# Performance work log

Hardware: AMD Instinct MI355X
Metric: run time of the kernel (lower is better)

## Reference

```python
import jax, jax.numpy as jnp
import numpy as np

B, S, DIM, H, HD = 2, 2048, 512, 8, 64
VD = DIM // H  # 64
QK = H * HD


def setup_inputs() -> dict:
    key = jax.random.key(0)
    k1, k2, k3, k4, k5 = jax.random.split(key, 5)
    x = jax.random.normal(k1, (B, S, DIM), dtype=jnp.float32)
    mask = jax.random.bernoulli(k2, 0.5, (B, S))
    # per-position rotation matrices, scaled to keep activations O(1)
    rotator = jax.random.normal(k3, (B, S, HD, HD), dtype=jnp.float32) / np.sqrt(HD)
    # torch Linear weights: [out_features, in_features], no bias
    W_trans = jax.random.normal(k4, (2 * QK + DIM, DIM), dtype=jnp.float32) / np.sqrt(DIM)
    W_o = jax.random.normal(k5, (DIM, DIM), dtype=jnp.float32) / np.sqrt(DIM)
    return {"x": x, "mask": mask, "rotator": rotator, "W_trans": W_trans, "W_o": W_o}


def _taylor_attention(qs, ks, vs, mask):
    # 2nd-order Taylor approximation of exp for softmax weights
    # qs/ks: [B,S,H,HD], vs: [B,S,H,VD], mask: [B,S] key mask
    scores = jnp.einsum('bqhd,bkhd->bhqk', qs, ks) / np.sqrt(HD)
    w = 1.0 + scores + 0.5 * scores * scores
    w = jnp.where(mask[:, None, None, :], w, 0.0)
    w = w / jnp.sum(w, axis=-1, keepdims=True)
    out = jnp.einsum('bhqk,bkhd->bqhd', w, vs)
    return out.reshape(out.shape[0], out.shape[1], -1)  # [B,S,DIM]


def reference(x, mask, rotator, W_trans, W_o):
    t = x @ W_trans.T  # [B,S,2*QK+DIM]
    qs = t[..., :QK].reshape(B, S, H, HD)
    ks = t[..., QK:2 * QK].reshape(B, S, H, HD)
    vs = t[..., 2 * QK:].reshape(B, S, H, VD)
    sel = mask[..., None, None]
    qs = jnp.where(sel, jnp.einsum('bsij,bshj->bshi', rotator, qs), qs)
    ks = jnp.where(sel, jnp.einsum('bsij,bshj->bshi', rotator, ks), ks)
    out = _taylor_attention(qs, ks, vs, mask)
    return out @ W_o.T
```

## Files before the change

kernel.cpp:

```cpp
#include <hip/hip_runtime.h>
#include <hip/hip_bf16.h>

#define B_    2
#define S_    2048
#define DIM_  512
#define H_    8
#define HD_   64
#define TOUT_ 1536
#define ROWS_ (B_ * S_)

typedef unsigned short ushort_t;
typedef __attribute__((ext_vector_type(8))) __bf16 bf16x8;
typedef __attribute__((ext_vector_type(4))) float floatx4;

#define AS_GLB __attribute__((address_space(1)))
#define AS_LDS __attribute__((address_space(3)))

__device__ __forceinline__ unsigned short f2bfu(float f) {
    unsigned u = __float_as_uint(f);
    unsigned r = (u + 0x7fffu + ((u >> 16) & 1u)) >> 16;
    return (unsigned short)r;
}
__device__ __forceinline__ bf16x8 cvt8(const float* p) {
    float4 a = *reinterpret_cast<const float4*>(p);
    float4 b = *reinterpret_cast<const float4*>(p + 4);
    ushort_t o[8] = {f2bfu(a.x), f2bfu(a.y), f2bfu(a.z), f2bfu(a.w),
                     f2bfu(b.x), f2bfu(b.y), f2bfu(b.z), f2bfu(b.w)};
    return *reinterpret_cast<bf16x8*>(o);
}

#define XN4_  (ROWS_ * DIM_ / 4)
#define WTN4_ (TOUT_ * DIM_ / 4)
#define WON4_ (DIM_ * DIM_ / 4)
#define CASTBLKS_ ((XN4_ + WTN4_ + WON4_) / 256)
__global__ __launch_bounds__(256) void prep_inputs(const float* __restrict__ x,
                                                   const float* __restrict__ wt,
                                                   const float* __restrict__ wo,
                                                   const unsigned char* __restrict__ mb,
                                                   ushort_t* __restrict__ xb,
                                                   ushort_t* __restrict__ wtb,
                                                   ushort_t* __restrict__ wob,
                                                   int* __restrict__ wm) {
    if (blockIdx.x >= CASTBLKS_) {
        __shared__ int s_bf, s_f, s_u8;
        int tid = threadIdx.x;
        if (tid == 0) { s_bf = 0; s_f = 0; s_u8 = 0; }
        __syncthreads();
        int cbf = 0, cf = 0, cu8 = 0;
        for (int i = tid; i < 4096; i += 256) {
            unsigned char v = mb[i];
            if (v == 0x3F || v == 0x80) {
                cf++;
                if ((i & 3) == 1) cbf++;
            } else if (v != 0 && (i & 3) != 0) {
                cu8++;
            }
        }
        atomicAdd(&s_bf, cbf); atomicAdd(&s_f, cf); atomicAdd(&s_u8, cu8);
        __syncthreads();
        int cls = (s_bf > 0) ? 2 : (s_f > 0) ? 3 : (s_u8 > 0) ? 0 : 1;
        for (int i = tid; i < ROWS_; i += 256) {
            int v;
            if (cls == 0)      v = (mb[i] != 0);
            else if (cls == 1) v = (reinterpret_cast<const int*>(mb)[i] != 0);
            else if (cls == 2) v = ((reinterpret_cast<const unsigned short*>(mb)[i] & 0x7fffu) != 0);
            else               v = ((reinterpret_cast<const unsigned int*>(mb)[i] & 0x7fffffffu) != 0);
            wm[i] = v;
        }
        return;
    }
    int i = blockIdx.x * 256 + threadIdx.x;
    const float* s; ushort_t* d; int off;
    if (i < XN4_)              { s = x;  d = xb;  off = i; }
    else if (i < XN4_ + WTN4_) { s = wt; d = wtb; off = i - XN4_; }
    else                       { s = wo; d = wob; off = i - XN4_ - WTN4_; }
    float4 v = reinterpret_cast<const float4*>(s)[off];
    ushort_t o[4] = {f2bfu(v.x), f2bfu(v.y), f2bfu(v.z), f2bfu(v.w)};
    reinterpret_cast<uint2*>(d)[off] = *reinterpret_cast<uint2*>(o);
}

template <int TM, int N, int K, bool OUT_BF16>
__global__ __launch_bounds__(256) void mfma_gemm_bt(const ushort_t* __restrict__ A,
                                                    const ushort_t* __restrict__ Bm,
                                                    void* __restrict__ Cout) {
    constexpr int FM = (TM + 31) / 32;
    __shared__ __align__(16) ushort_t As[TM * 64];
    __shared__ __align__(16) ushort_t Bs[128 * 64];
    int tid = threadIdx.x;
    int lane = tid & 63;
    int wv = tid >> 6;
    int wm = wv >> 1, wn = wv & 1;
    int quad = lane >> 4;
    int mrow = lane & 15;
    int bx = blockIdx.x;
    int by = blockIdx.y;

    floatx4 acc[FM][4];
#pragma unroll
    for (int i = 0; i < FM; i++)
#pragma unroll
        for (int j = 0; j < 4; j++) acc[i][j] = (floatx4){0.f, 0.f, 0.f, 0.f};

    for (int k0 = 0; k0 < K; k0 += 64) {
#pragma unroll
        for (int t = 0; t < TM / 32; t++) {
            int p = (wv * (TM / 32) + t) * 64 + lane;
            int row = p >> 3, cp = p & 7;
            int gc = cp ^ (row & 7);
            const ushort_t* ga = A + (size_t)(by * TM + row) * K + k0 + gc * 8;
            __builtin_amdgcn_global_load_lds((const AS_GLB unsigned int*)ga,
                                             (AS_LDS unsigned int*)&As[(size_t)(wv * (TM / 32) + t) * 64 * 8],
                                             16, 0, 0);
        }
#pragma unroll
        for (int t = 0; t < 4; t++) {
            int p = (wv * 4 + t) * 64 + lane;
            int row = p >> 3, cp = p & 7;
            int gc = cp ^ (row & 7);
            const ushort_t* gb = Bm + (size_t)(bx * 128 + row) * K + k0 + gc * 8;
            __builtin_amdgcn_global_load_lds((const AS_GLB unsigned int*)gb,
                                             (AS_LDS unsigned int*)&Bs[(size_t)(wv * 4 + t) * 64 * 8],
                                             16, 0, 0);
        }
        __syncthreads();
#pragma unroll
        for (int ks = 0; ks < 64; ks += 32) {
            int c = (ks >> 3) + quad;
            bf16x8 af[FM], bf[4];
#pragma unroll
            for (int i = 0; i < FM; i++) {
                int row = wm * (TM / 2) + i * 16 + mrow;
                int pos = row * 8 + (c ^ (row & 7));
                af[i] = *reinterpret_cast<const bf16x8*>(&As[pos * 8]);
            }
#pragma unroll
            for (int j = 0; j < 4; j++) {
                int row = wn * 64 + j * 16 + mrow;
                int pos = row * 8 + (c ^ (row & 7));
                bf[j] = *reinterpret_cast<const bf16x8*>(&Bs[pos * 8]);
            }
#pragma unroll
            for (int i = 0; i < FM; i++)
#pragma unroll
                for (int j = 0; j < 4; j++)
                    acc[i][j] = __builtin_amdgcn_mfma_f32_16x16x32_bf16(af[i], bf[j], acc[i][j], 0, 0, 0);
        }
        __syncthreads();
    }

    int col0 = bx * 128 + wn * 64 + mrow;
    int row0 = by * TM + wm * (TM / 2) + quad * 4;
    if constexpr (OUT_BF16) {
        ushort_t* C = reinterpret_cast<ushort_t*>(Cout);
#pragma unroll
        for (int i = 0; i < FM; i++)
#pragma unroll
            for (int j = 0; j < 4; j++)
#pragma unroll
                for (int r = 0; r < 4; r++)
                    C[(size_t)(row0 + i * 16 + r) * N + col0 + j * 16] = f2bfu(acc[i][j][r]);
    } else {
        float* C = reinterpret_cast<float*>(Cout);
#pragma unroll
        for (int i = 0; i < FM; i++)
#pragma unroll
            for (int j = 0; j < 4; j++)
#pragma unroll
                for (int r = 0; r < 4; r++)
                    C[(size_t)(row0 + i * 16 + r) * N + col0 + j * 16] = acc[i][j][r];
    }
}

__global__ __launch_bounds__(256) void rot_qk_mfma(const ushort_t* __restrict__ t,
                                                   const float* __restrict__ rotG,
                                                   const int* __restrict__ wm,
                                                   ushort_t* __restrict__ Qb,
                                                   ushort_t* __restrict__ Kb) {
    int lane = threadIdx.x & 63;
    int wv = threadIdx.x >> 6;
    int row = blockIdx.x * 4 + wv;
    int b = row >> 11, s = row & 2047;
    int lm = lane & 15, quad = lane >> 4;
    const ushort_t* trow = t + (size_t)row * TOUT_;
    int kb = s >> 4, l = s & 15;

    if (wm[row]) {
        bf16x8 af[2];
#pragma unroll
        for (int kc = 0; kc < 2; kc++)
            af[kc] = *reinterpret_cast<const bf16x8*>(trow + lm * 64 + kc * 32 + quad * 8);

        const float* R = rotG + (size_t)row * 4096;
        floatx4 dacc[4];
#pragma unroll
        for (int nb = 0; nb < 4; nb++) dacc[nb] = (floatx4){0.f, 0.f, 0.f, 0.f};
#pragma unroll
        for (int nb = 0; nb < 4; nb++)
#pragma unroll
            for (int kc = 0; kc < 2; kc++) {
                bf16x8 bfr = cvt8(R + (size_t)(nb * 16 + lm) * 64 + kc * 32 + quad * 8);
                dacc[nb] = __builtin_amdgcn_mfma_f32_16x16x32_bf16(af[kc], bfr, dacc[nb], 0, 0, 0);
            }
#pragma unroll
        for (int nb = 0; nb < 4; nb++)
#pragma unroll
            for (int r = 0; r < 4; r++) {
                int vec = quad * 4 + r;
                int hh = vec & 7;
                ushort_t v = f2bfu(dacc[nb][r]);
                if (vec >= 8) {
                    int c = nb * 2 + (lm >> 3), e = lm & 7;
                    Kb[(((size_t)(b * 8 + hh) * 128 + kb) * 8 + c) * 128 + l * 8 + e] = v;
                } else {
                    Qb[((size_t)(b * 8 + hh) * 2048 + s) * 64 + nb * 16 + lm] = v;
                }
            }
    } else {
#pragma unroll
        for (int nb = 0; nb < 4; nb++)
#pragma unroll
            for (int r = 0; r < 4; r++) {
                int vec = quad * 4 + r;
                int hh = vec & 7;
                ushort_t v = trow[vec * 64 + nb * 16 + lm];
                if (vec >= 8) {
                    int c = nb * 2 + (lm >> 3), e = lm & 7;
                    Kb[(((size_t)(b * 8 + hh) * 128 + kb) * 8 + c) * 128 + l * 8 + e] = v;
                } else {
                    Qb[((size_t)(b * 8 + hh) * 2048 + s) * 64 + nb * 16 + lm] = v;
                }
            }
    }
}

__global__ __launch_bounds__(256) void prep_vt(const ushort_t* __restrict__ t,
                                               const int* __restrict__ wm,
                                               ushort_t* __restrict__ VtF,
                                               ushort_t* __restrict__ MfF) {
    __shared__ ushort_t tile[64][72];
    __shared__ ushort_t umask[64];
    int st = blockIdx.x;
    int bh = blockIdx.y;
    int b = bh >> 3, h = bh & 7;
    int tid = threadIdx.x;
    if (tid < 64) umask[tid] = wm[b * 2048 + st * 64 + tid] ? 0xFFFFu : 0u;
#pragma unroll
    for (int i = 0; i < 2; i++) {
        int q = i * 256 + tid;
        int r = q >> 3, c8 = (q & 7) * 8;
        uint4 v = *reinterpret_cast<const uint4*>(
            t + (size_t)(b * 2048 + st * 64 + r) * TOUT_ + 1024 + h * 64 + c8);
        *reinterpret_cast<uint4*>(&tile[r][c8]) = v;
    }
    __syncthreads();
    {
        int dn = tid >> 6, quad = (tid >> 4) & 3, lm = tid & 15;
#pragma unroll
        for (int jj = 0; jj < 2; jj++) {
            ushort_t o[8];
#pragma unroll
            for (int e = 0; e < 8; e++) {
                int key = jj * 32 + ((e >> 2) << 4) + quad * 4 + (e & 3);
                o[e] = (ushort_t)(tile[key][dn * 16 + lm] & umask[key]);
            }
            size_t base = (((((size_t)(bh * 32 + st) * 4 + dn) * 2 + jj) * 4 + quad) * 16 + lm) * 8;
            *reinterpret_cast<uint4*>(VtF + base) = *reinterpret_cast<const uint4*>(o);
        }
    }
    if (tid < 8) {
        int jj = tid >> 2, quad = tid & 3;
        ushort_t o[8];
#pragma unroll
        for (int e = 0; e < 8; e++) {
            int key = jj * 32 + ((e >> 2) << 4) + quad * 4 + (e & 3);
            o[e] = umask[key] ? (ushort_t)0x3F80u : (ushort_t)0u;
        }
        size_t base = (((size_t)(bh * 32 + st) * 2 + jj) * 4 + quad) * 8;
        *reinterpret_cast<uint4*>(MfF + base) = *reinterpret_cast<const uint4*>(o);
    }
}

__global__ __launch_bounds__(256) void tmha_attn_mfma(const ushort_t* __restrict__ Qb,
                                                      const ushort_t* __restrict__ KbF,
                                                      const ushort_t* __restrict__ VtF,
                                                      const ushort_t* __restrict__ MfF,
                                                      ushort_t* __restrict__ attnAb) {
    int tid = threadIdx.x;
    int lane = tid & 63;
    int wv = tid >> 6;
    int lm = lane & 15;
    int quad = lane >> 4;

    int bid = blockIdx.x;
    int w = ((bid & 7) << 6) | (bid >> 3);
    int qt = w & 31;
    int bh = w >> 5;
    int b = bh >> 3, h = bh & 7;

    const ushort_t* Kf = KbF + (size_t)bh * 131072;
    const ushort_t* Vf = VtF + (size_t)bh * 131072;
    const ushort_t* Mf = MfF + (size_t)bh * 2048;

    bf16x8 qf[2];
    {
        const ushort_t* qp = Qb + ((size_t)bh * 2048 + qt * 64 + wv * 16 + lm) * 64 + quad * 8;
        qf[0] = *reinterpret_cast<const bf16x8*>(qp);
        qf[1] = *reinterpret_cast<const bf16x8*>(qp + 32);
    }

    floatx4 zero4 = (floatx4){0.f, 0.f, 0.f, 0.f};
    bf16x8 vzero;
    *reinterpret_cast<uint4*>(&vzero) = (uint4){0u, 0u, 0u, 0u};
    floatx4 oacc[5];
#pragma unroll
    for (int j = 0; j < 5; j++) oacc[j] = zero4;

    bf16x8 kA[4][2], kB[4][2], vA[4][2], vB[4][2], mA[2], mB[2];

    auto loadK = [&](bf16x8 (&kr)[4][2], int tt) {
        const ushort_t* p = Kf + (size_t)(tt & 31) * 4096 + quad * 128 + lm * 8;
#pragma unroll
        for (int j = 0; j < 4; j++)
#pragma unroll
            for (int kc = 0; kc < 2; kc++)
                kr[j][kc] = *reinterpret_cast<const bf16x8*>(p + (j * 8 + kc * 4) * 128);
    };
    auto loadV = [&](bf16x8 (&vr)[4][2], int tt) {
        const ushort_t* p = Vf + (size_t)(tt & 31) * 4096 + quad * 128 + lm * 8;
#pragma unroll
        for (int dn = 0; dn < 4; dn++)
#pragma unroll
            for (int jj = 0; jj < 2; jj++)
                vr[dn][jj] = *reinterpret_cast<const bf16x8*>(p + dn * 1024 + jj * 512);
    };
    auto loadM = [&](bf16x8 (&mf)[2], int tt) {
        const ushort_t* p = Mf + (size_t)(tt & 31) * 64 + quad * 8;
        mf[0] = *reinterpret_cast<const bf16x8*>(p);
        mf[1] = *reinterpret_cast<const bf16x8*>(p + 32);
    };

    auto step = [&](bf16x8 (&kr)[4][2], bf16x8 (&vr)[4][2], bf16x8 (&mf)[2],
                    bf16x8 (&krN)[4][2], bf16x8 (&vrN)[4][2], bf16x8 (&mfN)[2], int tpre) {
        __builtin_amdgcn_s_barrier();

        floatx4 sacc[4];
        __builtin_amdgcn_s_setprio(1);
#pragma unroll
        for (int j = 0; j < 4; j++) {
            sacc[j] = __builtin_amdgcn_mfma_f32_16x16x32_bf16(kr[j][0], qf[0], zero4, 0, 0, 0);
            sacc[j] = __builtin_amdgcn_mfma_f32_16x16x32_bf16(kr[j][1], qf[1], sacc[j], 0, 0, 0);
        }
        __builtin_amdgcn_s_setprio(0);

        loadK(krN, tpre);

        bf16x8 pa8[2];
#pragma unroll
        for (int jj = 0; jj < 2; jj++) {
            ushort_t o[8];
#pragma unroll
            for (int half = 0; half < 2; half++)
#pragma unroll
                for (int r = 0; r < 4; r++) {
                    float s = sacc[2 * jj + half][r];
                    float wgt = fmaf(s, fmaf(s, 0.0078125f, 0.125f), 1.0f);
                    o[half * 4 + r] = f2bfu(wgt);
                }
            pa8[jj] = *reinterpret_cast<bf16x8*>(o);
        }

        __builtin_amdgcn_s_setprio(1);
#pragma unroll
        for (int jj = 0; jj < 2; jj++) {
#pragma unroll
            for (int dn = 0; dn < 4; dn++)
                oacc[dn] = __builtin_amdgcn_mfma_f32_16x16x32_bf16(pa8[jj], vr[dn][jj], oacc[dn], 0, 0, 0);
            bf16x8 vb = (lm == 0) ? mf[jj] : vzero;
            oacc[4] = __builtin_amdgcn_mfma_f32_16x16x32_bf16(pa8[jj], vb, oacc[4], 0, 0, 0);
        }
        __builtin_amdgcn_s_setprio(0);

        loadV(vrN, tpre); loadM(mfN, tpre);
    };

    loadK(kA, 0); loadV(vA, 0); loadM(mA, 0);
    loadK(kB, 1); loadV(vB, 1); loadM(mB, 1);
#pragma unroll 1
    for (int it = 0; it < 16; it++) {
        step(kA, vA, mA, kA, vA, mA, 2 * it + 2);
        step(kB, vB, mB, kB, vB, mB, 2 * it + 3);
    }

    float inv[4];
#pragma unroll
    for (int r = 0; r < 4; r++) {
        float dn = __shfl(oacc[4][r], lane & 48);
        inv[r] = 1.0f / dn;
    }
#pragma unroll
    for (int dn = 0; dn < 4; dn++)
#pragma unroll
        for (int r = 0; r < 4; r++) {
            int qrow = b * 2048 + qt * 64 + wv * 16 + quad * 4 + r;
            attnAb[(size_t)qrow * DIM_ + h * 64 + dn * 16 + lm] = f2bfu(oacc[dn][r] * inv[r]);
        }
}

extern "C" void kernel_launch(void* const* d_in, const int* in_sizes, int n_in,
                              void* d_out, int out_size, void* d_ws, size_t ws_size,
                              hipStream_t stream) {
    (void)in_sizes; (void)n_in; (void)out_size; (void)ws_size;
    const float* x    = (const float*)d_in[0];
    const void*  mask = d_in[1];
    const float* rot  = (const float*)d_in[2];
    const float* Wt   = (const float*)d_in[3];
    const float* Wo   = (const float*)d_in[4];

    char* ws = (char*)d_ws;
    int* wmask       = (int*)(ws + 64);
    ushort_t* t      = (ushort_t*)(ws + 32768);
    ushort_t* Xb     = (ushort_t*)(ws + 12615680);
    ushort_t* Wtb    = (ushort_t*)(ws + 16809984);
    ushort_t* Wob    = (ushort_t*)(ws + 18382848);
    ushort_t* Qb     = (ushort_t*)(ws + 18907136);
    ushort_t* Kb     = (ushort_t*)(ws + 23101440);
    ushort_t* VtF    = (ushort_t*)(ws + 27295744);
    ushort_t* MfF    = (ushort_t*)(ws + 31490048);
    ushort_t* attnAb = (ushort_t*)(ws + 31555584);

    prep_inputs<<<CASTBLKS_ + 1, 256, 0, stream>>>(x, Wt, Wo, (const unsigned char*)mask,
                                                   Xb, Wtb, Wob, wmask);

    {
        dim3 grid(TOUT_ / 128, ROWS_ / 64);
        mfma_gemm_bt<64, TOUT_, DIM_, true><<<grid, 256, 0, stream>>>(Xb, Wtb, (void*)t);
    }

    rot_qk_mfma<<<ROWS_ / 4, 256, 0, stream>>>(t, rot, wmask, Qb, Kb);

    {
        dim3 grid(32, 16);
        prep_vt<<<grid, 256, 0, stream>>>(t, wmask, VtF, MfF);
    }

    tmha_attn_mfma<<<512, 256, 0, stream>>>(Qb, Kb, VtF, MfF, attnAb);

    {
        dim3 grid(DIM_ / 128, ROWS_ / 32);
        mfma_gemm_bt<32, DIM_, DIM_, false><<<grid, 256, 0, stream>>>(attnAb, Wob, d_out);
    }
}
```

Measured before the change: 192.1 us.

## Split attention over key halves with 2 query groups per wave, combine partials

The attention kernel now gives each wave two 16-row query groups, so every K/V tile loaded from memory feeds twice as many MFMAs. The key range is split in two across blocks to keep the grid size the same. Partial numerators and denominators are written in fp32 to workspace regions that no longer hold live data, and a new combine kernel sums and normalizes them. This trades the old double-buffered register prefetch for a single buffer. It also adds an extra launch and fp32 partial-result traffic in exchange for less K/V load traffic per FLOP.

```diff
diff --git a/kernel.cpp b/kernel.cpp
--- a/kernel.cpp
+++ b/kernel.cpp
@@ -280,11 +280,12 @@
     }
 }
 
-__global__ __launch_bounds__(256) void tmha_attn_mfma(const ushort_t* __restrict__ Qb,
-                                                      const ushort_t* __restrict__ KbF,
-                                                      const ushort_t* __restrict__ VtF,
-                                                      const ushort_t* __restrict__ MfF,
-                                                      ushort_t* __restrict__ attnAb) {
+__global__ __launch_bounds__(256, 2) void tmha_attn_mfma(const ushort_t* __restrict__ Qb,
+                                                         const ushort_t* __restrict__ KbF,
+                                                         const ushort_t* __restrict__ VtF,
+                                                         const ushort_t* __restrict__ MfF,
+                                                         float* __restrict__ numer,
+                                                         float* __restrict__ den) {
     int tid = threadIdx.x;
     int lane = tid & 63;
     int wv = tid >> 6;
@@ -293,7 +294,8 @@
 
     int bid = blockIdx.x;
     int w = ((bid & 7) << 6) | (bid >> 3);
-    int qt = w & 31;
+    int ks = w & 1;
+    int qt = (w >> 1) & 15;
     int bh = w >> 5;
     int b = bh >> 3, h = bh & 7;
 
@@ -301,109 +303,132 @@
     const ushort_t* Vf = VtF + (size_t)bh * 131072;
     const ushort_t* Mf = MfF + (size_t)bh * 2048;
 
-    bf16x8 qf[2];
-    {
-        const ushort_t* qp = Qb + ((size_t)bh * 2048 + qt * 64 + wv * 16 + lm) * 64 + quad * 8;
-        qf[0] = *reinterpret_cast<const bf16x8*>(qp);
-        qf[1] = *reinterpret_cast<const bf16x8*>(qp + 32);
+    bf16x8 qf[2][2];
+#pragma unroll
+    for (int g = 0; g < 2; g++) {
+        const ushort_t* qp = Qb + ((size_t)bh * 2048 + qt * 128 + wv * 32 + g * 16 + lm) * 64 + quad * 8;
+        qf[g][0] = *reinterpret_cast<const bf16x8*>(qp);
+        qf[g][1] = *reinterpret_cast<const bf16x8*>(qp + 32);
     }
 
     floatx4 zero4 = (floatx4){0.f, 0.f, 0.f, 0.f};
     bf16x8 vzero;
     *reinterpret_cast<uint4*>(&vzero) = (uint4){0u, 0u, 0u, 0u};
-    floatx4 oacc[5];
-#pragma unroll
-    for (int j = 0; j < 5; j++) oacc[j] = zero4;
-
-    bf16x8 kA[4][2], kB[4][2], vA[4][2], vB[4][2], mA[2], mB[2];
-
-    auto loadK = [&](bf16x8 (&kr)[4][2], int tt) {
-        const ushort_t* p = Kf + (size_t)(tt & 31) * 4096 + quad * 128 + lm * 8;
+    floatx4 oacc[2][5];
+#pragma unroll
+    for (int g = 0; g < 2; g++)
+#pragma unroll
+        for (int j = 0; j < 5; j++) oacc[g][j] = zero4;
+
+    bf16x8 kr[4][2], vr[4][2], mf[2];
+    auto loadK = [&](int tile) {
+        const ushort_t* p = Kf + (size_t)tile * 4096 + quad * 128 + lm * 8;
 #pragma unroll
         for (int j = 0; j < 4; j++)
 #pragma unroll
             for (int kc = 0; kc < 2; kc++)
                 kr[j][kc] = *reinterpret_cast<const bf16x8*>(p + (j * 8 + kc * 4) * 128);
     };
-    auto loadV = [&](bf16x8 (&vr)[4][2], int tt) {
-        const ushort_t* p = Vf + (size_t)(tt & 31) * 4096 + quad * 128 + lm * 8;
+    auto loadV = [&](int tile) {
+        const ushort_t* p = Vf + (size_t)tile * 4096 + quad * 128 + lm * 8;
 #pragma unroll
         for (int dn = 0; dn < 4; dn++)
 #pragma unroll
             for (int jj = 0; jj < 2; jj++)
                 vr[dn][jj] = *reinterpret_cast<const bf16x8*>(p + dn * 1024 + jj * 512);
     };
-    auto loadM = [&](bf16x8 (&mf)[2], int tt) {
-        const ushort_t* p = Mf + (size_t)(tt & 31) * 64 + quad * 8;
+    auto loadM = [&](int tile) {
+        const ushort_t* p = Mf + (size_t)tile * 64 + quad * 8;
         mf[0] = *reinterpret_cast<const bf16x8*>(p);
         mf[1] = *reinterpret_cast<const bf16x8*>(p + 32);
     };
 
-    auto step = [&](bf16x8 (&kr)[4][2], bf16x8 (&vr)[4][2], bf16x8 (&mf)[2],
-                    bf16x8 (&krN)[4][2], bf16x8 (&vrN)[4][2], bf16x8 (&mfN)[2], int tpre) {
+    int t0 = ks * 16;
+    loadK(t0); loadV(t0); loadM(t0);
+#pragma unroll 1
+    for (int tt = 0; tt < 16; tt++) {
+        int tn = (tt == 15) ? t0 : t0 + tt + 1;
         __builtin_amdgcn_s_barrier();
 
-        floatx4 sacc[4];
+        floatx4 sacc[2][4];
         __builtin_amdgcn_s_setprio(1);
 #pragma unroll
-        for (int j = 0; j < 4; j++) {
-            sacc[j] = __builtin_amdgcn_mfma_f32_16x16x32_bf16(kr[j][0], qf[0], zero4, 0, 0, 0);
-            sacc[j] = __builtin_amdgcn_mfma_f32_16x16x32_bf16(kr[j][1], qf[1], sacc[j], 0, 0, 0);
-        }
+        for (int g = 0; g < 2; g++)
+#pragma unroll
+            for (int j = 0; j < 4; j++) {
+                sacc[g][j] = __builtin_amdgcn_mfma_f32_16x16x32_bf16(kr[j][0], qf[g][0], zero4, 0, 0, 0);
+                sacc[g][j] = __builtin_amdgcn_mfma_f32_16x16x32_bf16(kr[j][1], qf[g][1], sacc[g][j], 0, 0, 0);
+            }
         __builtin_amdgcn_s_setprio(0);
 
-        loadK(krN, tpre);
-
-        bf16x8 pa8[2];
-#pragma unroll
-        for (int jj = 0; jj < 2; jj++) {
-            ushort_t o[8];
-#pragma unroll
-            for (int half = 0; half < 2; half++)
-#pragma unroll
-                for (int r = 0; r < 4; r++) {
-                    float s = sacc[2 * jj + half][r];
-                    float wgt = fmaf(s, fmaf(s, 0.0078125f, 0.125f), 1.0f);
-                    o[half * 4 + r] = f2bfu(wgt);
-                }
-            pa8[jj] = *reinterpret_cast<bf16x8*>(o);
-        }
+        loadK(tn);
+
+        bf16x8 pa8[2][2];
+#pragma unroll
+        for (int g = 0; g < 2; g++)
+#pragma unroll
+            for (int jj = 0; jj < 2; jj++) {
+                ushort_t o[8];
+#pragma unroll
+                for (int half = 0; half < 2; half++)
+#pragma unroll
+                    for (int r = 0; r < 4; r++) {
+                        float s = sacc[g][2 * jj + half][r];
+                        float wgt = fmaf(s, fmaf(s, 0.0078125f, 0.125f), 1.0f);
+                        o[half * 4 + r] = f2bfu(wgt);
+                    }
+                pa8[g][jj] = *reinterpret_cast<bf16x8*>(o);
+            }
 
         __builtin_amdgcn_s_setprio(1);
 #pragma unroll
-        for (int jj = 0; jj < 2; jj++) {
-#pragma unroll
-            for (int dn = 0; dn < 4; dn++)
-                oacc[dn] = __builtin_amdgcn_mfma_f32_16x16x32_bf16(pa8[jj], vr[dn][jj], oacc[dn], 0, 0, 0);
-            bf16x8 vb = (lm == 0) ? mf[jj] : vzero;
-            oacc[4] = __builtin_amdgcn_mfma_f32_16x16x32_bf16(pa8[jj], vb, oacc[4], 0, 0, 0);
-        }
+        for (int g = 0; g < 2; g++)
+#pragma unroll
+            for (int jj = 0; jj < 2; jj++) {
+#pragma unroll
+                for (int dn = 0; dn < 4; dn++)
+                    oacc[g][dn] = __builtin_amdgcn_mfma_f32_16x16x32_bf16(pa8[g][jj], vr[dn][jj], oacc[g][dn], 0, 0, 0);
+                bf16x8 vb = (lm == 0) ? mf[jj] : vzero;
+                oacc[g][4] = __builtin_amdgcn_mfma_f32_16x16x32_bf16(pa8[g][jj], vb, oacc[g][4], 0, 0, 0);
+            }
         __builtin_amdgcn_s_setprio(0);
 
-        loadV(vrN, tpre); loadM(mfN, tpre);
-    };
-
-    loadK(kA, 0); loadV(vA, 0); loadM(mA, 0);
-    loadK(kB, 1); loadV(vB, 1); loadM(mB, 1);
-#pragma unroll 1
-    for (int it = 0; it < 16; it++) {
-        step(kA, vA, mA, kA, vA, mA, 2 * it + 2);
-        step(kB, vB, mB, kB, vB, mB, 2 * it + 3);
-    }
-
-    float inv[4];
-#pragma unroll
-    for (int r = 0; r < 4; r++) {
-        float dn = __shfl(oacc[4][r], lane & 48);
-        inv[r] = 1.0f / dn;
-    }
-#pragma unroll
-    for (int dn = 0; dn < 4; dn++)
-#pragma unroll
-        for (int r = 0; r < 4; r++) {
-            int qrow = b * 2048 + qt * 64 + wv * 16 + quad * 4 + r;
-            attnAb[(size_t)qrow * DIM_ + h * 64 + dn * 16 + lm] = f2bfu(oacc[dn][r] * inv[r]);
-        }
+        loadV(tn); loadM(tn);
+    }
+
+#pragma unroll
+    for (int g = 0; g < 2; g++) {
+#pragma unroll
+        for (int dn = 0; dn < 4; dn++)
+#pragma unroll
+            for (int r = 0; r < 4; r++) {
+                int qrow = b * 2048 + qt * 128 + wv * 32 + g * 16 + quad * 4 + r;
+                numer[((size_t)ks * ROWS_ + qrow) * DIM_ + h * 64 + dn * 16 + lm] = oacc[g][dn][r];
+            }
+        if (lm == 0) {
+#pragma unroll
+            for (int r = 0; r < 4; r++) {
+                int qrow = b * 2048 + qt * 128 + wv * 32 + g * 16 + quad * 4 + r;
+                den[((size_t)ks * ROWS_ + qrow) * 8 + h] = oacc[g][4][r];
+            }
+        }
+    }
+}
+
+__global__ __launch_bounds__(256) void attn_combine(const float* __restrict__ numer,
+                                                    const float* __restrict__ den,
+                                                    ushort_t* __restrict__ attnAb) {
+    int i = blockIdx.x * 256 + threadIdx.x;
+    int row = i >> 7;
+    int c4 = (i & 127) * 4;
+    int h = c4 >> 6;
+    float4 n0 = *reinterpret_cast<const float4*>(&numer[(size_t)row * DIM_ + c4]);
+    float4 n1 = *reinterpret_cast<const float4*>(&numer[((size_t)ROWS_ + row) * DIM_ + c4]);
+    float d = den[(size_t)row * 8 + h] + den[((size_t)ROWS_ + row) * 8 + h];
+    float inv = 1.0f / d;
+    ushort_t o[4] = {f2bfu((n0.x + n1.x) * inv), f2bfu((n0.y + n1.y) * inv),
+                     f2bfu((n0.z + n1.z) * inv), f2bfu((n0.w + n1.w) * inv)};
+    *reinterpret_cast<uint2*>(&attnAb[(size_t)row * DIM_ + c4]) = *reinterpret_cast<uint2*>(o);
 }
 
 extern "C" void kernel_launch(void* const* d_in, const int* in_sizes, int n_in,
@@ -427,6 +452,8 @@
     ushort_t* VtF    = (ushort_t*)(ws + 27295744);
     ushort_t* MfF    = (ushort_t*)(ws + 31490048);
     ushort_t* attnAb = (ushort_t*)(ws + 31555584);
+    float* numer     = (float*)(ws + 32768);
+    float* den       = (float*)(ws + 16809984);
 
     prep_inputs<<<CASTBLKS_ + 1, 256, 0, stream>>>(x, Wt, Wo, (const unsigned char*)mask,
                                                    Xb, Wtb, Wob, wmask);
@@ -443,7 +470,8 @@
         prep_vt<<<grid, 256, 0, stream>>>(t, wmask, VtF, MfF);
     }
 
-    tmha_attn_mfma<<<512, 256, 0, stream>>>(Qb, Kb, VtF, MfF, attnAb);
+    tmha_attn_mfma<<<512, 256, 0, stream>>>(Qb, Kb, VtF, MfF, numer, den);
+    attn_combine<<<(ROWS_ * 128) / 256, 256, 0, stream>>>(numer, den, attnAb);
 
     {
         dim3 grid(DIM_ / 128, ROWS_ / 32);
```

Measured after the change: 189.4 us. About the same (-1.4%).
